# Kernel optimization log

Hardware: AMD Instinct MI355X
Metric: run time of the kernel (lower is better)

Reference implementation:

```python
import jax, jax.numpy as jnp
import numpy as np

BS, NS, S = 4, 16384, 8
C_PLANE, RES = 64, 128
IN_DIM = 3 * C_PLANE  # 192


def _bilerp(plane, uv):
    """plane: [B,C,H,W]; uv: [B,n,2] in [0,1] -> [B,n,C] bilinear samples (border clamp)."""
    B, C, H, W = plane.shape
    x = jnp.clip(uv[..., 0], 0.0, 1.0) * (W - 1)
    y = jnp.clip(uv[..., 1], 0.0, 1.0) * (H - 1)
    x0 = jnp.floor(x).astype(jnp.int32)
    y0 = jnp.floor(y).astype(jnp.int32)
    x1 = jnp.minimum(x0 + 1, W - 1)
    y1 = jnp.minimum(y0 + 1, H - 1)
    wx = (x - x0)[:, :, None]
    wy = (y - y0)[:, :, None]
    gat = jax.vmap(lambda p, yy, xx: p[:, yy, xx].T)  # per-batch gather -> [n,C]
    f00 = gat(plane, y0, x0)
    f01 = gat(plane, y0, x1)
    f10 = gat(plane, y1, x0)
    f11 = gat(plane, y1, x1)
    return (f00 * (1 - wx) * (1 - wy) + f01 * wx * (1 - wy)
            + f10 * (1 - wx) * wy + f11 * wx * wy)


def _sample_triplane(p, feat_xz, feat_xy, feat_yz):
    """p: [B,n,3] -> concat of bilinear samples from the three planes: [B,n,3C]."""
    f_xz = _bilerp(feat_xz, p[..., jnp.array([0, 2])])
    f_xy = _bilerp(feat_xy, p[..., jnp.array([0, 1])])
    f_yz = _bilerp(feat_yz, p[..., jnp.array([1, 2])])
    return jnp.concatenate([f_xz, f_xy, f_yz], axis=-1)


def setup_inputs() -> dict:
    key = jax.random.key(0)
    ks = jax.random.split(key, 12)
    w = 0.05  # small init so predicted offsets stay near the query point
    return {
        "query_pos": jax.random.uniform(ks[0], (BS, NS, 3), dtype=jnp.float32),
        "feat_xz": jax.random.normal(ks[1], (BS, C_PLANE, RES, RES), dtype=jnp.float32),
        "feat_xy": jax.random.normal(ks[2], (BS, C_PLANE, RES, RES), dtype=jnp.float32),
        "feat_yz": jax.random.normal(ks[3], (BS, C_PLANE, RES, RES), dtype=jnp.float32),
        "W_v": jax.random.normal(ks[4], (IN_DIM, IN_DIM), dtype=jnp.float32) * w,
        "b_v": jnp.zeros((IN_DIM,), jnp.float32),
        "W_out": jax.random.normal(ks[5], (IN_DIM, IN_DIM), dtype=jnp.float32) * w,
        "b_out": jnp.zeros((IN_DIM,), jnp.float32),
        "W_off": jax.random.normal(ks[6], (3 * S, IN_DIM), dtype=jnp.float32) * w,
        "b_off": jnp.zeros((3 * S,), jnp.float32),
        "W_wt": jax.random.normal(ks[7], (S, IN_DIM), dtype=jnp.float32) * w,
        "b_wt": jnp.zeros((S,), jnp.float32),
    }


def reference(query_pos, feat_xz, feat_xy, feat_yz, W_v, b_v, W_out, b_out,
              W_off, b_off, W_wt, b_wt):
    bs, ns, _ = query_pos.shape
    # feature at query points: [bs, ns, IN_DIM]
    feature = _sample_triplane(query_pos, feat_xz, feat_xy, feat_yz)
    # predicted per-sample offsets and weights
    off = (feature @ W_off.T + b_off).reshape(bs, ns, S, 3)
    wt = (feature @ W_wt.T + b_wt)[..., None]            # [bs, ns, S, 1]
    pts = off + query_pos[:, :, None, :]                  # [bs, ns, S, 3]
    # gather features at offset locations: [bs, ns*S, IN_DIM]
    aux = _sample_triplane(pts.reshape(bs, ns * S, 3), feat_xz, feat_xy, feat_yz)
    v = (aux @ W_v.T + b_v).reshape(bs, ns, S, -1)        # [bs, ns, S, hidden]
    out = (v * wt).sum(axis=-2)                           # weighted sum over samples
    out = out @ W_out.T + b_out + feature                 # residual add
    return out  # [bs, ns, IN_DIM]
```

## Files before the change

### kernel.cpp

```cpp
#include <hip/hip_runtime.h>

#define BS 4
#define NS 16384
#define S_SAMP 8
#define CPL 64
#define RES 128
#define IN_DIM 192
#define NPTS (BS * NS)
#define PL_STRIDE (RES * RES * CPL)
#define PLANES_T_FLOATS (BS * 3 * PL_STRIDE)

__global__ __launch_bounds__(256) void transpose_planes(
    const float* __restrict__ xz, const float* __restrict__ xy,
    const float* __restrict__ yz, float* __restrict__ T) {
  __shared__ float tile[64][33];
  int blk = blockIdx.x;
  int xt = blk & 3;
  int y  = (blk >> 2) & 127;
  int pl = (blk >> 9) % 3;
  int b  = blk / 1536;
  const float* src = (pl == 0) ? xz : ((pl == 1) ? xy : yz);
  src += (size_t)b * CPL * RES * RES + (size_t)y * RES + xt * 32;
  int tid = threadIdx.x;
  int xl = tid & 31, c0 = tid >> 5;
#pragma unroll
  for (int r = 0; r < 8; ++r) {
    int c = c0 + (r << 3);
    tile[c][xl] = src[(size_t)c * RES * RES + xl];
  }
  __syncthreads();
  float* dst = T + ((size_t)(b * 3 + pl) * RES * RES + (size_t)y * RES + xt * 32) * CPL;
  int c2 = tid & 63, x0 = tid >> 6;
#pragma unroll
  for (int r = 0; r < 8; ++r) {
    int xl2 = x0 + (r << 2);
    dst[(size_t)xl2 * CPL + c2] = tile[c2][xl2];
  }
}

__global__ __launch_bounds__(192) void precompute_wc(
    const float* __restrict__ W_v, const float* __restrict__ b_v,
    const float* __restrict__ W_out, float* __restrict__ WcT,
    float* __restrict__ bc) {
  int j = threadIdx.x;
  int k = blockIdx.x;
  if (k < IN_DIM) {
    float acc = 0.f;
    for (int m = 0; m < IN_DIM; ++m)
      acc += W_out[j * IN_DIM + m] * W_v[m * IN_DIM + k];
    WcT[k * IN_DIM + j] = acc;
  } else {
    float acc = 0.f;
    for (int m = 0; m < IN_DIM; ++m)
      acc += W_out[j * IN_DIM + m] * b_v[m];
    bc[j] = acc;
  }
}

__device__ __forceinline__ float bilerp(const float* __restrict__ pb, float u,
                                        float v, int lane) {
  u = fminf(fmaxf(u, 0.f), 1.f) * 127.f;
  v = fminf(fmaxf(v, 0.f), 1.f) * 127.f;
  float xf = floorf(u), yf = floorf(v);
  int x0 = (int)xf, y0 = (int)yf;
  int x1 = min(x0 + 1, 127), y1 = min(y0 + 1, 127);
  float wx = u - xf, wy = v - yf;
  float f00 = pb[(y0 * RES + x0) * CPL + lane];
  float f01 = pb[(y0 * RES + x1) * CPL + lane];
  float f10 = pb[(y1 * RES + x0) * CPL + lane];
  float f11 = pb[(y1 * RES + x1) * CPL + lane];
  return f00 * (1.f - wx) * (1.f - wy) + f01 * wx * (1.f - wy) +
         f10 * (1.f - wx) * wy + f11 * wx * wy;
}

__global__ __launch_bounds__(256) void fused_sample(
    const float* __restrict__ qpos, const float* __restrict__ planesT,
    const float* __restrict__ W_off, const float* __restrict__ b_off,
    const float* __restrict__ W_wt, const float* __restrict__ b_wt,
    float* __restrict__ waux, float* __restrict__ swtg,
    float* __restrict__ featg) {
  __shared__ float feat_lds[4][IN_DIM];
  __shared__ float offwt[4][32];
  int w = threadIdx.x >> 6, lane = threadIdx.x & 63;
  int p = (blockIdx.x << 2) + w;
  int b = p >> 14;
  float qx = qpos[p * 3 + 0], qy = qpos[p * 3 + 1], qz = qpos[p * 3 + 2];
  const float* Tb = planesT + (size_t)b * 3 * PL_STRIDE;

  float f0 = bilerp(Tb, qx, qz, lane);
  float f1 = bilerp(Tb + PL_STRIDE, qx, qy, lane);
  float f2 = bilerp(Tb + 2 * PL_STRIDE, qy, qz, lane);
  feat_lds[w][lane] = f0;
  feat_lds[w][64 + lane] = f1;
  feat_lds[w][128 + lane] = f2;
  __syncthreads();

  if (lane < 32) {
    const float* row;
    float bias;
    if (lane < 24) { row = W_off + lane * IN_DIM; bias = b_off[lane]; }
    else           { row = W_wt + (lane - 24) * IN_DIM; bias = b_wt[lane - 24]; }
    const float4* r4 = (const float4*)row;
    float a0 = 0.f, a1 = 0.f, a2 = 0.f, a3 = 0.f;
#pragma unroll 4
    for (int k4 = 0; k4 < IN_DIM / 4; ++k4) {
      float4 rv = r4[k4];
      a0 += rv.x * feat_lds[w][4 * k4 + 0];
      a1 += rv.y * feat_lds[w][4 * k4 + 1];
      a2 += rv.z * feat_lds[w][4 * k4 + 2];
      a3 += rv.w * feat_lds[w][4 * k4 + 3];
    }
    offwt[w][lane] = bias + ((a0 + a1) + (a2 + a3));
  }
  __syncthreads();

  float wa0 = 0.f, wa1 = 0.f, wa2 = 0.f, swt = 0.f;
#pragma unroll 2
  for (int s = 0; s < S_SAMP; ++s) {
    float wt = offwt[w][24 + s];
    float px = qx + offwt[w][3 * s + 0];
    float py = qy + offwt[w][3 * s + 1];
    float pz = qz + offwt[w][3 * s + 2];
    wa0 += wt * bilerp(Tb, px, pz, lane);
    wa1 += wt * bilerp(Tb + PL_STRIDE, px, py, lane);
    wa2 += wt * bilerp(Tb + 2 * PL_STRIDE, py, pz, lane);
    swt += wt;
  }

  size_t o = (size_t)p * IN_DIM + lane;
  waux[o] = wa0; waux[o + 64] = wa1; waux[o + 128] = wa2;
  if (lane == 0) swtg[p] = swt;
  featg[o] = f0; featg[o + 64] = f1; featg[o + 128] = f2;
}

__global__ __launch_bounds__(512) void out_gemm(
    const float* __restrict__ waux, const float* __restrict__ swtg,
    const float* __restrict__ WcT, const float* __restrict__ bc,
    const float* __restrict__ b_out, float* __restrict__ out) {
  __shared__ float wtile[64 * IN_DIM];
  int tid = threadIdx.x;
  int w = tid >> 6, lane = tid & 63;
  int pbase = blockIdx.x * 32 + w * 4;

  const float* wrow[4];
#pragma unroll
  for (int q = 0; q < 4; ++q)
    wrow[q] = waux + (size_t)__builtin_amdgcn_readfirstlane(pbase + q) * IN_DIM;

  float acc[4][3] = {};
  for (int c = 0; c < 3; ++c) {
#pragma unroll
    for (int r = 0; r < 24; ++r)
      wtile[tid + r * 512] = WcT[c * 64 * IN_DIM + tid + r * 512];
    __syncthreads();
#pragma unroll 2
    for (int k = 0; k < 64; ++k) {
      float v0 = wtile[k * IN_DIM + lane];
      float v1 = wtile[k * IN_DIM + 64 + lane];
      float v2 = wtile[k * IN_DIM + 128 + lane];
#pragma unroll
      for (int q = 0; q < 4; ++q) {
        float wv = wrow[q][c * 64 + k];
        acc[q][0] += v0 * wv;
        acc[q][1] += v1 * wv;
        acc[q][2] += v2 * wv;
      }
    }
    __syncthreads();
  }
#pragma unroll
  for (int q = 0; q < 4; ++q) {
    int p = pbase + q;
    float sw = swtg[p];
#pragma unroll
    for (int t = 0; t < 3; ++t) {
      int j = lane + t * 64;
      size_t o = (size_t)p * IN_DIM + j;
      out[o] = acc[q][t] + sw * bc[j] + b_out[j] + out[o];
    }
  }
}

extern "C" void kernel_launch(void* const* d_in, const int* in_sizes, int n_in,
                              void* d_out, int out_size, void* d_ws,
                              size_t ws_size, hipStream_t stream) {
  const float* qpos  = (const float*)d_in[0];
  const float* xz    = (const float*)d_in[1];
  const float* xy    = (const float*)d_in[2];
  const float* yz    = (const float*)d_in[3];
  const float* W_v   = (const float*)d_in[4];
  const float* b_v   = (const float*)d_in[5];
  const float* W_out = (const float*)d_in[6];
  const float* b_out = (const float*)d_in[7];
  const float* W_off = (const float*)d_in[8];
  const float* b_off = (const float*)d_in[9];
  const float* W_wt  = (const float*)d_in[10];
  const float* b_wt  = (const float*)d_in[11];

  float* ws      = (float*)d_ws;
  float* planesT = ws;
  float* waux    = planesT + PLANES_T_FLOATS;
  float* swtg    = waux + (size_t)NPTS * IN_DIM;
  float* WcT     = swtg + NPTS;
  float* bc      = WcT + IN_DIM * IN_DIM;
  float* out     = (float*)d_out;

  hipLaunchKernelGGL(transpose_planes, dim3(BS * 3 * RES * 4), dim3(256), 0,
                     stream, xz, xy, yz, planesT);
  hipLaunchKernelGGL(precompute_wc, dim3(IN_DIM + 1), dim3(IN_DIM), 0, stream,
                     W_v, b_v, W_out, WcT, bc);
  hipLaunchKernelGGL(fused_sample, dim3(NPTS / 4), dim3(256), 0, stream, qpos,
                     planesT, W_off, b_off, W_wt, b_wt, waux, swtg, out);
  hipLaunchKernelGGL(out_gemm, dim3(NPTS / 32), dim3(512), 0, stream, waux,
                     swtg, WcT, bc, b_out, out);
}
```

Measured before the change: 515.8 us.

## Scalarize bilinear indices, split offset GEMV across wave, enlarge out_gemm point tile

In the sampler, the bilinear corner indices are made wave-uniform with readfirstlane so addressing becomes scalar, and the interpolation is rewritten as lerps. The offset/weight projection now uses all 64 lanes, with each half covering half of K and the halves combined by a shuffle. Occupancy hints are added to the sampler. out_gemm now handles 128 points per block (16 per wave), so each LDS weight tile is reused across 4x more points, at the cost of more accumulator registers and a smaller grid.

Result: faster. 484.6 us (-6.1%).

```diff
diff --git a/kernel.cpp b/kernel.cpp
--- a/kernel.cpp
+++ b/kernel.cpp
@@ -57,23 +57,27 @@
   }
 }
 
-__device__ __forceinline__ float bilerp(const float* __restrict__ pb, float u,
-                                        float v, int lane) {
+__device__ __forceinline__ float bilerp_s(const float* __restrict__ pb, float u,
+                                          float v, int lane) {
   u = fminf(fmaxf(u, 0.f), 1.f) * 127.f;
   v = fminf(fmaxf(v, 0.f), 1.f) * 127.f;
   float xf = floorf(u), yf = floorf(v);
-  int x0 = (int)xf, y0 = (int)yf;
-  int x1 = min(x0 + 1, 127), y1 = min(y0 + 1, 127);
   float wx = u - xf, wy = v - yf;
-  float f00 = pb[(y0 * RES + x0) * CPL + lane];
-  float f01 = pb[(y0 * RES + x1) * CPL + lane];
-  float f10 = pb[(y1 * RES + x0) * CPL + lane];
-  float f11 = pb[(y1 * RES + x1) * CPL + lane];
-  return f00 * (1.f - wx) * (1.f - wy) + f01 * wx * (1.f - wy) +
-         f10 * (1.f - wx) * wy + f11 * wx * wy;
-}
-
-__global__ __launch_bounds__(256) void fused_sample(
+  int x0 = __builtin_amdgcn_readfirstlane((int)xf);
+  int y0 = __builtin_amdgcn_readfirstlane((int)yf);
+  int dx = (x0 < 127) ? CPL : 0;
+  int dy = (y0 < 127) ? RES * CPL : 0;
+  const float* b00 = pb + (((y0 << 7) + x0) << 6);
+  float f00 = b00[lane];
+  float f01 = b00[dx + lane];
+  float f10 = b00[dy + lane];
+  float f11 = b00[dy + dx + lane];
+  float fx0 = f00 + wx * (f01 - f00);
+  float fx1 = f10 + wx * (f11 - f10);
+  return fx0 + wy * (fx1 - fx0);
+}
+
+__global__ __launch_bounds__(256, 4) void fused_sample(
     const float* __restrict__ qpos, const float* __restrict__ planesT,
     const float* __restrict__ W_off, const float* __restrict__ b_off,
     const float* __restrict__ W_wt, const float* __restrict__ b_wt,
@@ -87,43 +91,46 @@
   float qx = qpos[p * 3 + 0], qy = qpos[p * 3 + 1], qz = qpos[p * 3 + 2];
   const float* Tb = planesT + (size_t)b * 3 * PL_STRIDE;
 
-  float f0 = bilerp(Tb, qx, qz, lane);
-  float f1 = bilerp(Tb + PL_STRIDE, qx, qy, lane);
-  float f2 = bilerp(Tb + 2 * PL_STRIDE, qy, qz, lane);
+  float f0 = bilerp_s(Tb, qx, qz, lane);
+  float f1 = bilerp_s(Tb + PL_STRIDE, qx, qy, lane);
+  float f2 = bilerp_s(Tb + 2 * PL_STRIDE, qy, qz, lane);
   feat_lds[w][lane] = f0;
   feat_lds[w][64 + lane] = f1;
   feat_lds[w][128 + lane] = f2;
   __syncthreads();
 
-  if (lane < 32) {
-    const float* row;
-    float bias;
-    if (lane < 24) { row = W_off + lane * IN_DIM; bias = b_off[lane]; }
-    else           { row = W_wt + (lane - 24) * IN_DIM; bias = b_wt[lane - 24]; }
-    const float4* r4 = (const float4*)row;
+  {
+    int oj = lane & 31;
+    const float* row = (oj < 24) ? (W_off + oj * IN_DIM)
+                                 : (W_wt + (oj - 24) * IN_DIM);
+    float bias = (oj < 24) ? b_off[oj] : b_wt[oj - 24];
+    int k0 = (lane >> 5) * 96;
+    const float4* r4 = (const float4*)(row + k0);
     float a0 = 0.f, a1 = 0.f, a2 = 0.f, a3 = 0.f;
+#pragma unroll
+    for (int k4 = 0; k4 < 24; ++k4) {
+      float4 rv = r4[k4];
+      a0 += rv.x * feat_lds[w][k0 + 4 * k4 + 0];
+      a1 += rv.y * feat_lds[w][k0 + 4 * k4 + 1];
+      a2 += rv.z * feat_lds[w][k0 + 4 * k4 + 2];
+      a3 += rv.w * feat_lds[w][k0 + 4 * k4 + 3];
+    }
+    float acc = (a0 + a1) + (a2 + a3);
+    acc += __shfl_xor(acc, 32);
+    if (lane < 32) offwt[w][oj] = acc + bias;
+  }
+  __syncthreads();
+
+  float wa0 = 0.f, wa1 = 0.f, wa2 = 0.f, swt = 0.f;
 #pragma unroll 4
-    for (int k4 = 0; k4 < IN_DIM / 4; ++k4) {
-      float4 rv = r4[k4];
-      a0 += rv.x * feat_lds[w][4 * k4 + 0];
-      a1 += rv.y * feat_lds[w][4 * k4 + 1];
-      a2 += rv.z * feat_lds[w][4 * k4 + 2];
-      a3 += rv.w * feat_lds[w][4 * k4 + 3];
-    }
-    offwt[w][lane] = bias + ((a0 + a1) + (a2 + a3));
-  }
-  __syncthreads();
-
-  float wa0 = 0.f, wa1 = 0.f, wa2 = 0.f, swt = 0.f;
-#pragma unroll 2
   for (int s = 0; s < S_SAMP; ++s) {
     float wt = offwt[w][24 + s];
     float px = qx + offwt[w][3 * s + 0];
     float py = qy + offwt[w][3 * s + 1];
     float pz = qz + offwt[w][3 * s + 2];
-    wa0 += wt * bilerp(Tb, px, pz, lane);
-    wa1 += wt * bilerp(Tb + PL_STRIDE, px, py, lane);
-    wa2 += wt * bilerp(Tb + 2 * PL_STRIDE, py, pz, lane);
+    wa0 += wt * bilerp_s(Tb, px, pz, lane);
+    wa1 += wt * bilerp_s(Tb + PL_STRIDE, px, py, lane);
+    wa2 += wt * bilerp_s(Tb + 2 * PL_STRIDE, py, pz, lane);
     swt += wt;
   }
 
@@ -140,45 +147,51 @@
   __shared__ float wtile[64 * IN_DIM];
   int tid = threadIdx.x;
   int w = tid >> 6, lane = tid & 63;
-  int pbase = blockIdx.x * 32 + w * 4;
-
-  const float* wrow[4];
-#pragma unroll
-  for (int q = 0; q < 4; ++q)
-    wrow[q] = waux + (size_t)__builtin_amdgcn_readfirstlane(pbase + q) * IN_DIM;
-
-  float acc[4][3] = {};
+  int p0 = blockIdx.x * 128 + w * 16;
+
+  float acc[4][4][3] = {};
   for (int c = 0; c < 3; ++c) {
 #pragma unroll
     for (int r = 0; r < 24; ++r)
       wtile[tid + r * 512] = WcT[c * 64 * IN_DIM + tid + r * 512];
     __syncthreads();
-#pragma unroll 2
-    for (int k = 0; k < 64; ++k) {
-      float v0 = wtile[k * IN_DIM + lane];
-      float v1 = wtile[k * IN_DIM + 64 + lane];
-      float v2 = wtile[k * IN_DIM + 128 + lane];
-#pragma unroll
-      for (int q = 0; q < 4; ++q) {
-        float wv = wrow[q][c * 64 + k];
-        acc[q][0] += v0 * wv;
-        acc[q][1] += v1 * wv;
-        acc[q][2] += v2 * wv;
+#pragma unroll
+    for (int g = 0; g < 4; ++g) {
+      const float* wrow[4];
+#pragma unroll
+      for (int q = 0; q < 4; ++q)
+        wrow[q] = waux +
+                  (size_t)__builtin_amdgcn_readfirstlane(p0 + g * 4 + q) * IN_DIM +
+                  c * 64;
+#pragma unroll 4
+      for (int k = 0; k < 64; ++k) {
+        float v0 = wtile[k * IN_DIM + lane];
+        float v1 = wtile[k * IN_DIM + 64 + lane];
+        float v2 = wtile[k * IN_DIM + 128 + lane];
+#pragma unroll
+        for (int q = 0; q < 4; ++q) {
+          float wv = wrow[q][k];
+          acc[g][q][0] += v0 * wv;
+          acc[g][q][1] += v1 * wv;
+          acc[g][q][2] += v2 * wv;
+        }
       }
     }
     __syncthreads();
   }
 #pragma unroll
-  for (int q = 0; q < 4; ++q) {
-    int p = pbase + q;
-    float sw = swtg[p];
-#pragma unroll
-    for (int t = 0; t < 3; ++t) {
-      int j = lane + t * 64;
-      size_t o = (size_t)p * IN_DIM + j;
-      out[o] = acc[q][t] + sw * bc[j] + b_out[j] + out[o];
+  for (int g = 0; g < 4; ++g)
+#pragma unroll
+    for (int q = 0; q < 4; ++q) {
+      int p = p0 + g * 4 + q;
+      float sw = swtg[p];
+#pragma unroll
+      for (int t = 0; t < 3; ++t) {
+        int j = lane + t * 64;
+        size_t o = (size_t)p * IN_DIM + j;
+        out[o] = acc[g][q][t] + sw * bc[j] + b_out[j] + out[o];
+      }
     }
-  }
 }
 
 extern "C" void kernel_launch(void* const* d_in, const int* in_sizes, int n_in,
@@ -211,6 +224,6 @@
                      W_v, b_v, W_out, WcT, bc);
   hipLaunchKernelGGL(fused_sample, dim3(NPTS / 4), dim3(256), 0, stream, qpos,
                      planesT, W_off, b_off, W_wt, b_wt, waux, swtg, out);
-  hipLaunchKernelGGL(out_gemm, dim3(NPTS / 32), dim3(512), 0, stream, waux,
+  hipLaunchKernelGGL(out_gemm, dim3(NPTS / 128), dim3(512), 0, stream, waux,
                      swtg, WcT, bc, b_out, out);
 }
```
